# Kernel tuning notes

Measured on AMD Instinct MI355X. Metric: run time of the kernel, lower is better.

## Reference

```python
import jax, jax.numpy as jnp
import numpy as np

B, S, D, H, DH = 2, 2048, 2048, 16, 128


def _rope(t, cos, sin):
    # t: [b,s,h,dh]; pairs are consecutive elements (view(..., -1, 2) in torch)
    te = t[..., 0::2]
    to = t[..., 1::2]
    re = te * cos - to * sin
    im = te * sin + to * cos
    return jnp.stack([re, im], axis=-1).reshape(t.shape)


def setup_inputs() -> dict:
    key = jax.random.key(0)
    ks = jax.random.split(key, 5)
    inv = 1.0 / np.sqrt(D)
    x = jax.random.normal(ks[0], (B, S, D), dtype=jnp.float32)
    # standard RoPE angle table -> cos/sin of shape [1,S,1,DH//2]
    pos = jnp.arange(S, dtype=jnp.float32)[:, None]
    freqs = 1.0 / (10000.0 ** (jnp.arange(0, DH, 2, dtype=jnp.float32) / DH))
    ang = pos * freqs[None, :]
    rope_cos = jnp.cos(ang)[None, :, None, :]
    rope_sin = jnp.sin(ang)[None, :, None, :]
    Wq = jax.random.normal(ks[1], (D, D), dtype=jnp.float32) * inv
    Wk = jax.random.normal(ks[2], (D, D), dtype=jnp.float32) * inv
    Wv = jax.random.normal(ks[3], (D, D), dtype=jnp.float32) * inv
    Wo = jax.random.normal(ks[4], (D, D), dtype=jnp.float32) * inv
    return {"x": x, "rope_cos": rope_cos, "rope_sin": rope_sin,
            "Wq": Wq, "Wk": Wk, "Wv": Wv, "Wo": Wo}


def reference(x, rope_cos, rope_sin, Wq, Wk, Wv, Wo):
    b, s, d = x.shape
    scale = DH ** (-0.5)
    # nn.Linear(bias=False): y = x @ W.T
    q = (x @ Wq.T).reshape(b, s, H, DH)
    k = (x @ Wk.T).reshape(b, s, H, DH)
    v = (x @ Wv.T).reshape(b, s, H, DH)
    q = _rope(q, rope_cos[:, :s], rope_sin[:, :s])
    k = _rope(k, rope_cos[:, :s], rope_sin[:, :s])
    q = q.transpose(0, 2, 1, 3)  # bhsd
    k = k.transpose(0, 2, 1, 3)
    v = v.transpose(0, 2, 1, 3)
    # full scores needed for softmax normalizer
    scores = jnp.einsum('bhqd,bhkd->bhqk', q, k) * scale
    lse = jax.nn.logsumexp(scores, axis=-1)  # [b,h,s]
    # torch.einsum('bhss,bhsd->bhsd', softmax(scores), v) takes the DIAGONAL
    # of the softmax matrix and scales v elementwise. Replicate exactly:
    diag = jnp.einsum('bhsd,bhsd->bhs', q, k) * scale  # scores[b,h,s,s]
    w = jnp.exp(diag - lse)  # softmax(scores)[b,h,s,s]
    out = w[..., None] * v  # [b,h,s,dh]
    out = out.transpose(0, 2, 1, 3).reshape(b, s, d)
    return out @ Wo.T
```

## Files before the change

### kernel.cpp

```cpp
#include <hip/hip_runtime.h>

#define B_  2
#define S_  2048
#define D_  2048
#define H_  16
#define DH_ 128
#define NQKV 6144

typedef __bf16 bf16;
typedef __bf16 bf16x2 __attribute__((ext_vector_type(2)));
typedef __bf16 bf16x4 __attribute__((ext_vector_type(4)));
typedef __bf16 bf16x8 __attribute__((ext_vector_type(8)));
typedef float  f32x4  __attribute__((ext_vector_type(4)));

#define EXP2F(x) __builtin_amdgcn_exp2f(x)
#define LOG2F(x) __builtin_amdgcn_logf(x)

static constexpr float kQScale = 0.08838834764831845f * 1.4426950408889634f;

__device__ __forceinline__ void async16(const void* g, void* l) {
  __builtin_amdgcn_global_load_lds(
      (const __attribute__((address_space(1))) void*)g,
      (__attribute__((address_space(3))) void*)l, 16, 0, 0);
}

__global__ void cvt_all(const float* __restrict__ x,  const float* __restrict__ wq,
                        const float* __restrict__ wk, const float* __restrict__ wv,
                        const float* __restrict__ wo,
                        bf16* __restrict__ xb, bf16* __restrict__ wqkv,
                        bf16* __restrict__ wob) {
  int bid = blockIdx.x;
  const float* s; bf16* d; int base;
  if (bid < 8192)        { s = x;  d = xb;             base = bid; }
  else if (bid < 12288)  { s = wq; d = wqkv;           base = bid - 8192; }
  else if (bid < 16384)  { s = wk; d = wqkv + 4194304; base = bid - 12288; }
  else if (bid < 20480)  { s = wv; d = wqkv + 8388608; base = bid - 16384; }
  else                   { s = wo; d = wob;            base = bid - 20480; }
  int i = (base * 256 + threadIdx.x) * 4;
  float4 v = *(const float4*)(s + i);
  bf16x4 o = {(bf16)v.x, (bf16)v.y, (bf16)v.z, (bf16)v.w};
  *(bf16x4*)(d + i) = o;
}

__global__ __launch_bounds__(256, 2) void gemm_qkv(
    const bf16* __restrict__ A, const bf16* __restrict__ Bm,
    const float* __restrict__ rc, const float* __restrict__ rs,
    bf16* __restrict__ C) {
  __shared__ alignas(16) bf16 As[2][128 * 32];
  __shared__ alignas(16) bf16 Bs[2][128 * 32];
  const int tid = threadIdx.x;
  const int lane = tid & 63;
  const int wv = tid >> 6;
  const int quad = lane >> 4, c16 = lane & 15;
  const int wm = (wv >> 1) * 64, wn = (wv & 1) * 64;
  const int m0 = blockIdx.y * 128, n0 = blockIdx.x * 128;

  const bf16* ag = A  + (size_t)(m0 + (tid >> 2)) * D_ + (tid & 3) * 8;
  const bf16* bg = Bm + (size_t)(n0 + (tid >> 2)) * D_ + (tid & 3) * 8;
  char* asl = (char*)As + tid * 16;
  char* bsl = (char*)Bs + tid * 16;

  f32x4 acc[4][4] = {};
  for (int k0 = 0; k0 < D_; k0 += 64) {
    __syncthreads();
    async16(ag + k0,                 asl);
    async16(ag + k0 + 64 * D_,       asl + 4096);
    async16(ag + k0 + 32,            asl + 8192);
    async16(ag + k0 + 32 + 64 * D_,  asl + 12288);
    async16(bg + k0,                 bsl);
    async16(bg + k0 + 64 * D_,       bsl + 4096);
    async16(bg + k0 + 32,            bsl + 8192);
    async16(bg + k0 + 32 + 64 * D_,  bsl + 12288);
    __syncthreads();
#pragma unroll
    for (int half = 0; half < 2; ++half) {
      bf16x8 af[4], bfr[4];
#pragma unroll
      for (int i = 0; i < 4; ++i)
        af[i] = *(const bf16x8*)(As[half] + (wm + i * 16 + c16) * 32 + quad * 8);
#pragma unroll
      for (int j = 0; j < 4; ++j)
        bfr[j] = *(const bf16x8*)(Bs[half] + (wn + j * 16 + c16) * 32 + quad * 8);
#pragma unroll
      for (int i = 0; i < 4; ++i)
#pragma unroll
        for (int j = 0; j < 4; ++j)
          acc[i][j] = __builtin_amdgcn_mfma_f32_16x16x32_bf16(af[i], bfr[j], acc[i][j], 0, 0, 0);
    }
  }

  if (n0 < 4096) {
    const float sc = (n0 < 2048) ? kQScale : 1.0f;
#pragma unroll
    for (int i = 0; i < 4; ++i) {
      const int gmi = m0 + wm + i * 16 + quad * 4;
#pragma unroll
      for (int j = 0; j < 4; ++j) {
        const int gn = n0 + wn + j * 16 + c16;
        const int d = gn & 127;
#pragma unroll
        for (int r = 0; r < 4; ++r) {
          float v = acc[i][j][r];
          float p = __shfl_xor(v, 1);
          const int gm = gmi + r;
          const int s = gm & 2047;
          const int si = s * 64 + (d >> 1);
          float c = rc[si], sn = rs[si];
          float re = (v * c - p * sn) * sc;
          float im = (v * sn + p * c) * sc;
          if (!(lane & 1)) {
            bf16x2 o = {(bf16)re, (bf16)im};
            *(bf16x2*)(C + (size_t)gm * NQKV + gn) = o;
          }
        }
      }
    }
  } else {
#pragma unroll
    for (int i = 0; i < 4; ++i) {
      const int gmi = m0 + wm + i * 16 + quad * 4;
#pragma unroll
      for (int j = 0; j < 4; ++j) {
        const int gn = n0 + wn + j * 16 + c16;
#pragma unroll
        for (int r = 0; r < 4; ++r) {
          float v = acc[i][j][r];
          float p = __shfl_xor(v, 1);
          if (!(lane & 1)) {
            bf16x2 o = {(bf16)v, (bf16)p};
            *(bf16x2*)(C + (size_t)(gmi + r) * NQKV + gn) = o;
          }
        }
      }
    }
  }
}

__global__ __launch_bounds__(256, 2) void score_wv(
    const bf16* __restrict__ qkv, bf16* __restrict__ t) {
  __shared__ alignas(16) bf16 Qs[4 * 128 * 32];
  __shared__ alignas(16) bf16 Ks[4 * 128 * 32];
  __shared__ float diagL[128];
  __shared__ float lseL[128];
  const int tid = threadIdx.x;
  const int lane = tid & 63, wv = tid >> 6;
  const int quad = lane >> 4, c16 = lane & 15;
  const int wm = wv * 32;
  const int bh = blockIdx.y;
  const int b = bh >> 4, h = bh & 15;
  const int m0 = blockIdx.x * 128;

  const bf16* qg = qkv + (size_t)(b * 2048 + m0 + (tid >> 2)) * NQKV
                 + h * 128 + (tid & 3) * 8;
  char* ql = (char*)Qs + tid * 16;
#pragma unroll
  for (int kt = 0; kt < 4; ++kt) {
    async16(qg + kt * 32,                     ql + kt * 8192);
    async16(qg + kt * 32 + (size_t)64 * NQKV, ql + kt * 8192 + 4096);
  }

  const bf16* kg = qkv + (size_t)(b * 2048 + (tid >> 2)) * NQKV
                 + 2048 + h * 128 + (tid & 3) * 8;
  char* kl = (char*)Ks + tid * 16;

  float sums[8] = {0.f, 0.f, 0.f, 0.f, 0.f, 0.f, 0.f, 0.f};

  for (int n0 = 0; n0 < S_; n0 += 128) {
    __syncthreads();
#pragma unroll
    for (int kt = 0; kt < 4; ++kt) {
      async16(kg + (size_t)n0 * NQKV + kt * 32,        kl + kt * 8192);
      async16(kg + (size_t)(n0 + 64) * NQKV + kt * 32, kl + kt * 8192 + 4096);
    }
    __syncthreads();
    f32x4 acc[2][8] = {};
#pragma unroll
    for (int kt = 0; kt < 4; ++kt) {
      bf16x8 a[2], bb[8];
#pragma unroll
      for (int i = 0; i < 2; ++i)
        a[i] = *(const bf16x8*)(Qs + kt * 4096 + (wm + i * 16 + c16) * 32 + quad * 8);
#pragma unroll
      for (int j = 0; j < 8; ++j)
        bb[j] = *(const bf16x8*)(Ks + kt * 4096 + (j * 16 + c16) * 32 + quad * 8);
#pragma unroll
      for (int i = 0; i < 2; ++i)
#pragma unroll
        for (int j = 0; j < 8; ++j)
          acc[i][j] = __builtin_amdgcn_mfma_f32_16x16x32_bf16(a[i], bb[j], acc[i][j], 0, 0, 0);
    }
    if (n0 == m0) {
#pragma unroll
      for (int i = 0; i < 2; ++i)
#pragma unroll
        for (int j = 0; j < 8; ++j)
          if (j == 2 * wv + i) {
#pragma unroll
            for (int r = 0; r < 4; ++r)
              if (c16 == quad * 4 + r)
                diagL[wm + i * 16 + quad * 4 + r] = acc[i][j][r];
          }
    }
#pragma unroll
    for (int i = 0; i < 2; ++i)
#pragma unroll
      for (int j = 0; j < 8; ++j)
#pragma unroll
        for (int r = 0; r < 4; ++r)
          sums[i * 4 + r] += EXP2F(acc[i][j][r]);
  }

#pragma unroll
  for (int tix = 0; tix < 8; ++tix) {
    float s = sums[tix];
    s += __shfl_xor(s, 1);
    s += __shfl_xor(s, 2);
    s += __shfl_xor(s, 4);
    s += __shfl_xor(s, 8);
    if (c16 == 0) {
      int i = tix >> 2, r = tix & 3;
      lseL[wm + i * 16 + quad * 4 + r] = LOG2F(s);
    }
  }

  __syncthreads();
  const int row = tid >> 1, ch = tid & 1;
  const float w = EXP2F(diagL[row] - lseL[row]);
  const size_t grow = (size_t)(b * 2048 + m0 + row);
  const bf16* vsrc = qkv + grow * NQKV + 4096 + h * 128 + ch * 64;
  bf16* tdst = t + grow * 2048 + h * 128 + ch * 64;
#pragma unroll
  for (int c = 0; c < 8; ++c) {
    bf16x8 vv = *(const bf16x8*)(vsrc + c * 8);
    bf16x8 oo;
#pragma unroll
    for (int r = 0; r < 8; ++r) oo[r] = (bf16)((float)vv[r] * w);
    *(bf16x8*)(tdst + c * 8) = oo;
  }
}

__global__ __launch_bounds__(256, 2) void gemm_out(
    const bf16* __restrict__ A, const bf16* __restrict__ Bm, float* __restrict__ C) {
  __shared__ alignas(16) bf16 As[2][128 * 32];
  __shared__ alignas(16) bf16 Bs[2][128 * 32];
  const int tid = threadIdx.x;
  const int lane = tid & 63, wv = tid >> 6;
  const int quad = lane >> 4, c16 = lane & 15;
  const int wm = (wv >> 1) * 64, wn = (wv & 1) * 64;
  const int m0 = blockIdx.y * 128, n0 = blockIdx.x * 128;

  const bf16* ag = A  + (size_t)(m0 + (tid >> 2)) * D_ + (tid & 3) * 8;
  const bf16* bg = Bm + (size_t)(n0 + (tid >> 2)) * D_ + (tid & 3) * 8;
  char* asl = (char*)As + tid * 16;
  char* bsl = (char*)Bs + tid * 16;

  f32x4 acc[4][4] = {};
  for (int k0 = 0; k0 < D_; k0 += 64) {
    __syncthreads();
    async16(ag + k0,                 asl);
    async16(ag + k0 + 64 * D_,       asl + 4096);
    async16(ag + k0 + 32,            asl + 8192);
    async16(ag + k0 + 32 + 64 * D_,  asl + 12288);
    async16(bg + k0,                 bsl);
    async16(bg + k0 + 64 * D_,       bsl + 4096);
    async16(bg + k0 + 32,            bsl + 8192);
    async16(bg + k0 + 32 + 64 * D_,  bsl + 12288);
    __syncthreads();
#pragma unroll
    for (int half = 0; half < 2; ++half) {
      bf16x8 af[4], bfr[4];
#pragma unroll
      for (int i = 0; i < 4; ++i)
        af[i] = *(const bf16x8*)(As[half] + (wm + i * 16 + c16) * 32 + quad * 8);
#pragma unroll
      for (int j = 0; j < 4; ++j)
        bfr[j] = *(const bf16x8*)(Bs[half] + (wn + j * 16 + c16) * 32 + quad * 8);
#pragma unroll
      for (int i = 0; i < 4; ++i)
#pragma unroll
        for (int j = 0; j < 4; ++j)
          acc[i][j] = __builtin_amdgcn_mfma_f32_16x16x32_bf16(af[i], bfr[j], acc[i][j], 0, 0, 0);
    }
  }
#pragma unroll
  for (int i = 0; i < 4; ++i)
#pragma unroll
    for (int j = 0; j < 4; ++j)
#pragma unroll
      for (int r = 0; r < 4; ++r) {
        float v = acc[i][j][r];
        float p = __shfl_xor(v, 1);
        if (!(lane & 1)) {
          int gm = m0 + wm + i * 16 + quad * 4 + r;
          int gn = n0 + wn + j * 16 + c16;
          float2 o = {v, p};
          *(float2*)(C + (size_t)gm * D_ + gn) = o;
        }
      }
}

extern "C" void kernel_launch(void* const* d_in, const int* in_sizes, int n_in,
                              void* d_out, int out_size, void* d_ws, size_t ws_size,
                              hipStream_t stream) {
  (void)in_sizes; (void)n_in; (void)out_size; (void)ws_size;
  const float* x  = (const float*)d_in[0];
  const float* rc = (const float*)d_in[1];
  const float* rs = (const float*)d_in[2];
  const float* Wq = (const float*)d_in[3];
  const float* Wk = (const float*)d_in[4];
  const float* Wv = (const float*)d_in[5];
  const float* Wo = (const float*)d_in[6];

  char* ws = (char*)d_ws;
  bf16* xb   = (bf16*)ws;
  bf16* wqkv = (bf16*)(ws + 16777216);
  bf16* wob  = (bf16*)(ws + 16777216 + 25165824);
  bf16* qkv  = (bf16*)(ws + 16777216 + 25165824 + 8388608);

  cvt_all<<<24576, 256, 0, stream>>>(x, Wq, Wk, Wv, Wo, xb, wqkv, wob);
  gemm_qkv<<<dim3(48, 32), 256, 0, stream>>>(xb, wqkv, rc, rs, qkv);
  score_wv<<<dim3(16, 32), 256, 0, stream>>>(qkv, xb );
  gemm_out<<<dim3(16, 32), 256, 0, stream>>>(xb, wob, (float*)d_out);
}
```

Before: 374.5 us.

## Restructure QKV GEMM into 256x256 tiles with 8-wave pipelined, swizzled LDS loads

The QKV projection GEMM moves from 128x128 tiles with 4 waves and a load-then-sync loop to 256x256 tiles with 8 waves. The new K loop uses double-buffered LDS with XOR-swizzled layout, interleaves async global-to-LDS loads for the next tile between four MFMA sub-phases, and uses explicit barriers, waitcnts and setprio. The goal is to hide memory latency behind MFMA work, cut LDS bank conflicts and raise data reuse per tile. In exchange the kernel uses more registers and LDS, and the grid drops to 384 blocks, which may underfill the CUs.

```diff
diff --git a/kernel.cpp b/kernel.cpp
--- a/kernel.cpp
+++ b/kernel.cpp
@@ -42,61 +42,136 @@
   *(bf16x4*)(d + i) = o;
 }
 
-__global__ __launch_bounds__(256, 2) void gemm_qkv(
+template<int IB, int JB>
+__device__ __forceinline__ void mfma_quad(f32x4 (&acc)[8][4],
+                                          const bf16x8 (&a)[4][2],
+                                          const bf16x8 (&b)[2][2]) {
+#pragma unroll
+  for (int i = 0; i < 4; ++i)
+#pragma unroll
+    for (int j = 0; j < 2; ++j) {
+      acc[IB + i][JB + j] = __builtin_amdgcn_mfma_f32_16x16x32_bf16(
+          a[i][0], b[j][0], acc[IB + i][JB + j], 0, 0, 0);
+      acc[IB + i][JB + j] = __builtin_amdgcn_mfma_f32_16x16x32_bf16(
+          a[i][1], b[j][1], acc[IB + i][JB + j], 0, 0, 0);
+    }
+}
+
+#define SBAR()  __builtin_amdgcn_s_barrier()
+#define LGKM0() asm volatile("s_waitcnt lgkmcnt(0)" ::: "memory")
+#define VMC2()  asm volatile("s_waitcnt vmcnt(2)" ::: "memory")
+
+__global__ __launch_bounds__(512, 2) void gemm_qkv(
     const bf16* __restrict__ A, const bf16* __restrict__ Bm,
     const float* __restrict__ rc, const float* __restrict__ rs,
     bf16* __restrict__ C) {
-  __shared__ alignas(16) bf16 As[2][128 * 32];
-  __shared__ alignas(16) bf16 Bs[2][128 * 32];
-  const int tid = threadIdx.x;
+  __shared__ alignas(16) bf16 As[2 * 256 * 64];
+  __shared__ alignas(16) bf16 Bs[2 * 256 * 64];
+  const int tid  = threadIdx.x;
   const int lane = tid & 63;
-  const int wv = tid >> 6;
+  const int wid  = tid >> 6;
+  const int wr   = wid >> 2, wc = wid & 3;
   const int quad = lane >> 4, c16 = lane & 15;
-  const int wm = (wv >> 1) * 64, wn = (wv & 1) * 64;
-  const int m0 = blockIdx.y * 128, n0 = blockIdx.x * 128;
-
-  const bf16* ag = A  + (size_t)(m0 + (tid >> 2)) * D_ + (tid & 3) * 8;
-  const bf16* bg = Bm + (size_t)(n0 + (tid >> 2)) * D_ + (tid & 3) * 8;
-  char* asl = (char*)As + tid * 16;
-  char* bsl = (char*)Bs + tid * 16;
-
-  f32x4 acc[4][4] = {};
-  for (int k0 = 0; k0 < D_; k0 += 64) {
-    __syncthreads();
-    async16(ag + k0,                 asl);
-    async16(ag + k0 + 64 * D_,       asl + 4096);
-    async16(ag + k0 + 32,            asl + 8192);
-    async16(ag + k0 + 32 + 64 * D_,  asl + 12288);
-    async16(bg + k0,                 bsl);
-    async16(bg + k0 + 64 * D_,       bsl + 4096);
-    async16(bg + k0 + 32,            bsl + 8192);
-    async16(bg + k0 + 32 + 64 * D_,  bsl + 12288);
-    __syncthreads();
-#pragma unroll
-    for (int half = 0; half < 2; ++half) {
-      bf16x8 af[4], bfr[4];
-#pragma unroll
-      for (int i = 0; i < 4; ++i)
-        af[i] = *(const bf16x8*)(As[half] + (wm + i * 16 + c16) * 32 + quad * 8);
-#pragma unroll
-      for (int j = 0; j < 4; ++j)
-        bfr[j] = *(const bf16x8*)(Bs[half] + (wn + j * 16 + c16) * 32 + quad * 8);
-#pragma unroll
-      for (int i = 0; i < 4; ++i)
-#pragma unroll
-        for (int j = 0; j < 4; ++j)
-          acc[i][j] = __builtin_amdgcn_mfma_f32_16x16x32_bf16(af[i], bfr[j], acc[i][j], 0, 0, 0);
-    }
+  const int m0 = blockIdx.y * 256, n0 = blockIdx.x * 256;
+
+  const int trow = tid >> 3;
+  const int tcol = ((tid & 7) ^ (trow & 7)) * 8;
+  const bf16* agS = A  + (size_t)(m0 + trow) * D_ + tcol;
+  const bf16* bgS = Bm + (size_t)(n0 + trow) * D_ + tcol;
+  char* asD = (char*)As + tid * 16;
+  char* bsD = (char*)Bs + tid * 16;
+
+  const int xorv  = (c16 & 7) << 4;
+  const int colh0 = (quad * 16) ^ xorv;
+  const char* aL = (const char*)As + (wr * 128 + c16) * 128 + colh0;
+  const char* aH = (const char*)As + (wr * 128 + c16) * 128 + (colh0 ^ 64);
+  const char* bL = (const char*)Bs + (wc * 64 + c16) * 128 + colh0;
+  const char* bH = (const char*)Bs + (wc * 64 + c16) * 128 + (colh0 ^ 64);
+
+  f32x4 acc[8][4] = {};
+
+  async16(agS,                 asD);
+  async16(agS +  64 * D_,      asD + 8192);
+  async16(agS + 128 * D_,      asD + 16384);
+  async16(agS + 192 * D_,      asD + 24576);
+  async16(bgS,                 bsD);
+  async16(bgS +  64 * D_,      bsD + 8192);
+  async16(bgS + 128 * D_,      bsD + 16384);
+  async16(bgS + 192 * D_,      bsD + 24576);
+  async16(agS + 64,            asD + 32768);
+  async16(agS + 64 * D_ + 64,  asD + 32768 + 8192);
+  VMC2();
+  SBAR();
+
+  for (int t = 0; t < 32; ++t) {
+    const int cb = (t & 1) << 15;
+    const int cx = cb ^ 32768;
+    const int k1 = (t < 31) ? (t + 1) * 64 : 0;
+    const int k2 = (t < 30) ? (t + 2) * 64 : 0;
+    bf16x8 a0[4][2], a1[4][2], b0[2][2], b1[2][2];
+
+#pragma unroll
+    for (int i = 0; i < 4; ++i) {
+      a0[i][0] = *(const bf16x8*)(aL + cb + i * 2048);
+      a0[i][1] = *(const bf16x8*)(aH + cb + i * 2048);
+    }
+#pragma unroll
+    for (int j = 0; j < 2; ++j) {
+      b0[j][0] = *(const bf16x8*)(bL + cb + j * 2048);
+      b0[j][1] = *(const bf16x8*)(bH + cb + j * 2048);
+    }
+    async16(agS + 128 * D_ + k1, asD + cx + 16384);
+    async16(agS + 192 * D_ + k1, asD + cx + 24576);
+    SBAR(); LGKM0();
+    __builtin_amdgcn_s_setprio(1);
+    mfma_quad<0, 0>(acc, a0, b0);
+    __builtin_amdgcn_s_setprio(0);
+    SBAR();
+
+#pragma unroll
+    for (int j = 0; j < 2; ++j) {
+      b1[j][0] = *(const bf16x8*)(bL + cb + (2 + j) * 2048);
+      b1[j][1] = *(const bf16x8*)(bH + cb + (2 + j) * 2048);
+    }
+    async16(bgS + k1,            bsD + cx);
+    async16(bgS + 64 * D_ + k1,  bsD + cx + 8192);
+    SBAR(); LGKM0();
+    __builtin_amdgcn_s_setprio(1);
+    mfma_quad<0, 2>(acc, a0, b1);
+    __builtin_amdgcn_s_setprio(0);
+    SBAR();
+
+#pragma unroll
+    for (int i = 0; i < 4; ++i) {
+      a1[i][0] = *(const bf16x8*)(aL + cb + (4 + i) * 2048);
+      a1[i][1] = *(const bf16x8*)(aH + cb + (4 + i) * 2048);
+    }
+    async16(bgS + 128 * D_ + k1, bsD + cx + 16384);
+    async16(bgS + 192 * D_ + k1, bsD + cx + 24576);
+    SBAR(); LGKM0();
+    __builtin_amdgcn_s_setprio(1);
+    mfma_quad<4, 0>(acc, a1, b0);
+    __builtin_amdgcn_s_setprio(0);
+    SBAR();
+
+    async16(agS + k2,            asD + cb);
+    async16(agS + 64 * D_ + k2,  asD + cb + 8192);
+    VMC2();
+    SBAR();
+    __builtin_amdgcn_s_setprio(1);
+    mfma_quad<4, 2>(acc, a1, b1);
+    __builtin_amdgcn_s_setprio(0);
+    SBAR();
   }
 
   if (n0 < 4096) {
     const float sc = (n0 < 2048) ? kQScale : 1.0f;
 #pragma unroll
-    for (int i = 0; i < 4; ++i) {
-      const int gmi = m0 + wm + i * 16 + quad * 4;
+    for (int i = 0; i < 8; ++i) {
+      const int gmi = m0 + wr * 128 + i * 16 + quad * 4;
 #pragma unroll
       for (int j = 0; j < 4; ++j) {
-        const int gn = n0 + wn + j * 16 + c16;
+        const int gn = n0 + wc * 64 + j * 16 + c16;
         const int d = gn & 127;
 #pragma unroll
         for (int r = 0; r < 4; ++r) {
@@ -105,9 +180,9 @@
           const int gm = gmi + r;
           const int s = gm & 2047;
           const int si = s * 64 + (d >> 1);
-          float c = rc[si], sn = rs[si];
-          float re = (v * c - p * sn) * sc;
-          float im = (v * sn + p * c) * sc;
+          float cz = rc[si], sn = rs[si];
+          float re = (v * cz - p * sn) * sc;
+          float im = (v * sn + p * cz) * sc;
           if (!(lane & 1)) {
             bf16x2 o = {(bf16)re, (bf16)im};
             *(bf16x2*)(C + (size_t)gm * NQKV + gn) = o;
@@ -117,11 +192,11 @@
     }
   } else {
 #pragma unroll
-    for (int i = 0; i < 4; ++i) {
-      const int gmi = m0 + wm + i * 16 + quad * 4;
+    for (int i = 0; i < 8; ++i) {
+      const int gmi = m0 + wr * 128 + i * 16 + quad * 4;
 #pragma unroll
       for (int j = 0; j < 4; ++j) {
-        const int gn = n0 + wn + j * 16 + c16;
+        const int gn = n0 + wc * 64 + j * 16 + c16;
 #pragma unroll
         for (int r = 0; r < 4; ++r) {
           float v = acc[i][j][r];
@@ -318,7 +393,7 @@
   bf16* qkv  = (bf16*)(ws + 16777216 + 25165824 + 8388608);
 
   cvt_all<<<24576, 256, 0, stream>>>(x, Wq, Wk, Wv, Wo, xb, wqkv, wob);
-  gemm_qkv<<<dim3(48, 32), 256, 0, stream>>>(xb, wqkv, rc, rs, qkv);
+  gemm_qkv<<<dim3(24, 16), 512, 0, stream>>>(xb, wqkv, rc, rs, qkv);
   score_wv<<<dim3(16, 32), 256, 0, stream>>>(qkv, xb );
   gemm_out<<<dim3(16, 32), 256, 0, stream>>>(xb, wob, (float*)d_out);
 }
```

Result: slower. 416.4 us (+11.2%).

## Keep Q in registers, XOR-swizzle K tile in LDS, shrink QKV GEMM k-step

Applied to the files above, without the earlier changes.

In the score kernel, Q fragments now load straight from global memory into registers once per block, so the Q shared-memory buffer goes away. K is staged as row-major 128x128 tiles with an XOR-swizzled 16-byte chunk layout, meant to avoid LDS bank conflicts on fragment reads, and each K fragment is consumed as soon as it is loaded. The QKV GEMM now steps k by 32 instead of 64 with half the LDS, which lowers LDS use but doubles the number of barriers per k loop.

```diff
diff --git a/kernel.cpp b/kernel.cpp
--- a/kernel.cpp
+++ b/kernel.cpp
@@ -46,8 +46,8 @@
     const bf16* __restrict__ A, const bf16* __restrict__ Bm,
     const float* __restrict__ rc, const float* __restrict__ rs,
     bf16* __restrict__ C) {
-  __shared__ alignas(16) bf16 As[2][128 * 32];
-  __shared__ alignas(16) bf16 Bs[2][128 * 32];
+  __shared__ alignas(16) bf16 As[128 * 32];
+  __shared__ alignas(16) bf16 Bs[128 * 32];
   const int tid = threadIdx.x;
   const int lane = tid & 63;
   const int wv = tid >> 6;
@@ -61,32 +61,25 @@
   char* bsl = (char*)Bs + tid * 16;
 
   f32x4 acc[4][4] = {};
-  for (int k0 = 0; k0 < D_; k0 += 64) {
-    __syncthreads();
-    async16(ag + k0,                 asl);
-    async16(ag + k0 + 64 * D_,       asl + 4096);
-    async16(ag + k0 + 32,            asl + 8192);
-    async16(ag + k0 + 32 + 64 * D_,  asl + 12288);
-    async16(bg + k0,                 bsl);
-    async16(bg + k0 + 64 * D_,       bsl + 4096);
-    async16(bg + k0 + 32,            bsl + 8192);
-    async16(bg + k0 + 32 + 64 * D_,  bsl + 12288);
-    __syncthreads();
-#pragma unroll
-    for (int half = 0; half < 2; ++half) {
-      bf16x8 af[4], bfr[4];
-#pragma unroll
-      for (int i = 0; i < 4; ++i)
-        af[i] = *(const bf16x8*)(As[half] + (wm + i * 16 + c16) * 32 + quad * 8);
+  for (int k0 = 0; k0 < D_; k0 += 32) {
+    __syncthreads();
+    async16(ag + k0,            asl);
+    async16(ag + k0 + 64 * D_,  asl + 4096);
+    async16(bg + k0,            bsl);
+    async16(bg + k0 + 64 * D_,  bsl + 4096);
+    __syncthreads();
+    bf16x8 af[4], bfr[4];
+#pragma unroll
+    for (int i = 0; i < 4; ++i)
+      af[i] = *(const bf16x8*)(As + (wm + i * 16 + c16) * 32 + quad * 8);
+#pragma unroll
+    for (int j = 0; j < 4; ++j)
+      bfr[j] = *(const bf16x8*)(Bs + (wn + j * 16 + c16) * 32 + quad * 8);
+#pragma unroll
+    for (int i = 0; i < 4; ++i)
 #pragma unroll
       for (int j = 0; j < 4; ++j)
-        bfr[j] = *(const bf16x8*)(Bs[half] + (wn + j * 16 + c16) * 32 + quad * 8);
-#pragma unroll
-      for (int i = 0; i < 4; ++i)
-#pragma unroll
-        for (int j = 0; j < 4; ++j)
-          acc[i][j] = __builtin_amdgcn_mfma_f32_16x16x32_bf16(af[i], bfr[j], acc[i][j], 0, 0, 0);
-    }
+        acc[i][j] = __builtin_amdgcn_mfma_f32_16x16x32_bf16(af[i], bfr[j], acc[i][j], 0, 0, 0);
   }
 
   if (n0 < 4096) {
@@ -138,8 +131,7 @@
 
 __global__ __launch_bounds__(256, 2) void score_wv(
     const bf16* __restrict__ qkv, bf16* __restrict__ t) {
-  __shared__ alignas(16) bf16 Qs[4 * 128 * 32];
-  __shared__ alignas(16) bf16 Ks[4 * 128 * 32];
+  __shared__ alignas(16) bf16 Ks[128 * 128];
   __shared__ float diagL[128];
   __shared__ float lseL[128];
   const int tid = threadIdx.x;
@@ -150,17 +142,21 @@
   const int b = bh >> 4, h = bh & 15;
   const int m0 = blockIdx.x * 128;
 
-  const bf16* qg = qkv + (size_t)(b * 2048 + m0 + (tid >> 2)) * NQKV
-                 + h * 128 + (tid & 3) * 8;
-  char* ql = (char*)Qs + tid * 16;
-#pragma unroll
-  for (int kt = 0; kt < 4; ++kt) {
-    async16(qg + kt * 32,                     ql + kt * 8192);
-    async16(qg + kt * 32 + (size_t)64 * NQKV, ql + kt * 8192 + 4096);
-  }
-
-  const bf16* kg = qkv + (size_t)(b * 2048 + (tid >> 2)) * NQKV
-                 + 2048 + h * 128 + (tid & 3) * 8;
+  bf16x8 qf[2][4];
+  {
+    const bf16* qbase = qkv + (size_t)(b * 2048 + m0 + wm + c16) * NQKV
+                      + h * 128 + quad * 8;
+#pragma unroll
+    for (int i = 0; i < 2; ++i)
+#pragma unroll
+      for (int kt = 0; kt < 4; ++kt)
+        qf[i][kt] = *(const bf16x8*)(qbase + (size_t)(i * 16) * NQKV + kt * 32);
+  }
+
+  const int srow = tid >> 4;
+  const int schunk = (tid & 15) ^ (srow & 7);
+  const bf16* kg = qkv + (size_t)(b * 2048 + srow) * NQKV
+                 + 2048 + h * 128 + schunk * 8;
   char* kl = (char*)Ks + tid * 16;
 
   float sums[8] = {0.f, 0.f, 0.f, 0.f, 0.f, 0.f, 0.f, 0.f};
@@ -168,26 +164,20 @@
   for (int n0 = 0; n0 < S_; n0 += 128) {
     __syncthreads();
 #pragma unroll
+    for (int i = 0; i < 8; ++i)
+      async16(kg + (size_t)(n0 + i * 16) * NQKV, kl + i * 4096);
+    __syncthreads();
+    f32x4 acc[2][8] = {};
+#pragma unroll
     for (int kt = 0; kt < 4; ++kt) {
-      async16(kg + (size_t)n0 * NQKV + kt * 32,        kl + kt * 8192);
-      async16(kg + (size_t)(n0 + 64) * NQKV + kt * 32, kl + kt * 8192 + 4096);
-    }
-    __syncthreads();
-    f32x4 acc[2][8] = {};
-#pragma unroll
-    for (int kt = 0; kt < 4; ++kt) {
-      bf16x8 a[2], bb[8];
-#pragma unroll
-      for (int i = 0; i < 2; ++i)
-        a[i] = *(const bf16x8*)(Qs + kt * 4096 + (wm + i * 16 + c16) * 32 + quad * 8);
-#pragma unroll
-      for (int j = 0; j < 8; ++j)
-        bb[j] = *(const bf16x8*)(Ks + kt * 4096 + (j * 16 + c16) * 32 + quad * 8);
-#pragma unroll
-      for (int i = 0; i < 2; ++i)
-#pragma unroll
-        for (int j = 0; j < 8; ++j)
-          acc[i][j] = __builtin_amdgcn_mfma_f32_16x16x32_bf16(a[i], bb[j], acc[i][j], 0, 0, 0);
+#pragma unroll
+      for (int j = 0; j < 8; ++j) {
+        bf16x8 bb = *(const bf16x8*)((const char*)Ks + (j * 16 + c16) * 256
+                        + ((((kt * 4 + quad) ^ (c16 & 7))) << 4));
+#pragma unroll
+        for (int i = 0; i < 2; ++i)
+          acc[i][j] = __builtin_amdgcn_mfma_f32_16x16x32_bf16(qf[i][kt], bb, acc[i][j], 0, 0, 0);
+      }
     }
     if (n0 == m0) {
 #pragma unroll
```

Result: slower. 386.4 us (+3.2%).
